# Kernel tuning notes

Measured on AMD Instinct MI355X. Metric: run time of the kernel, lower is better.

## Reference

```python
import jax, jax.numpy as jnp
import numpy as np

B, S, D, A, O = 4, 4096, 256, 64, 256

def setup_inputs() -> dict:
    key = jax.random.key(0)
    k1, k2, k3, k4, k5 = jax.random.split(key, 5)
    x = jax.random.normal(k1, (B, S, D), dtype=jnp.float32)
    # weights stored as [in, out] so projection is x @ W (same math as torch Linear W^T)
    Wk = jax.random.normal(k2, (D, A), dtype=jnp.float32) * (1.0 / np.sqrt(D))
    Wq = jax.random.normal(k3, (D, A), dtype=jnp.float32) * (1.0 / np.sqrt(D))
    Wv = jax.random.normal(k4, (D, A), dtype=jnp.float32) * (1.0 / np.sqrt(D))
    Wo = jax.random.normal(k5, (A, O), dtype=jnp.float32) * (1.0 / np.sqrt(A))
    return {"x": x, "Wk": Wk, "Wq": Wq, "Wv": Wv, "Wo": Wo}

def reference(x, Wk, Wq, Wv, Wo):
    # Single-head self-attention; dropout is identity at inference.
    k = x @ Wk  # [B,S,A]
    q = x @ Wq  # [B,S,A]
    v = x @ Wv  # [B,S,A]
    scale = 1.0 / jnp.sqrt(jnp.asarray(A, x.dtype))
    # logits[b,s,t] = k[b,s,:] . q[b,t,:]   (K @ Q^T in the torch code)
    logits = jnp.einsum('bsa,bta->bst', k, q) * scale
    w = jax.nn.softmax(logits, axis=-1)  # softmax over t
    # out[b,s,:] = sum_t w[b,s,t] * v[b,t,:]  (equivalent to V @ w^T then transpose)
    attn = jnp.einsum('bst,bta->bsa', w, v)
    return attn @ Wo  # [B,S,O]
```

## Files before the change

### kernel.cpp

```cpp
#include <hip/hip_runtime.h>


#define SQN 4096
#define AN 64
#define ON 256

typedef short bf16x8 __attribute__((ext_vector_type(8)));
typedef float f32x4 __attribute__((ext_vector_type(4)));

__device__ __forceinline__ unsigned short f2bf(float f) {
    unsigned int u = __float_as_uint(f);
    u += 0x7fffu + ((u >> 16) & 1u);
    return (unsigned short)(u >> 16);
}
__device__ __forceinline__ unsigned int cvtpk(float lo, float hi) {
    unsigned int r;
    asm("v_cvt_pk_bf16_f32 %0, %1, %2" : "=v"(r) : "v"(lo), "v"(hi));
    return r;
}
__device__ __forceinline__ float exp2_hw(float x) {
    float r; asm("v_exp_f32 %0, %1" : "=v"(r) : "v"(x)); return r;
}

__global__ __launch_bounds__(256) void k_wtrans(
    const float* __restrict__ Wk, const float* __restrict__ Wq,
    const float* __restrict__ Wv, const float* __restrict__ Wo,
    unsigned short* __restrict__ WT, unsigned short* __restrict__ WoT)
{
    int bidx = blockIdx.x, tid = threadIdx.x;
    if (bidx < 24) {
        int m = bidx >> 3, chunk = bidx & 7;
        const float* src = (m == 0) ? Wk : (m == 1) ? Wq : Wv;
        float scl = (m == 1) ? 0.18033688011112042f : 1.0f;
        unsigned short* dst = WT + (m * 64 + chunk * 8) * 256;
        for (int idx = tid; idx < 8 * 256; idx += 256) {
            int a = chunk * 8 + (idx >> 8), d = idx & 255;
            dst[idx] = f2bf(src[d * 64 + a] * scl);
        }
    } else {
        int chunk = bidx - 24;
        for (int idx = tid; idx < 32 * 64; idx += 256) {
            int o = chunk * 32 + (idx >> 6), a = idx & 63;
            WoT[o * 64 + a] = f2bf(Wo[a * 256 + o]);
        }
    }
}

__global__ __launch_bounds__(256) void k_proj(
    const float* __restrict__ x, const unsigned short* __restrict__ WT,
    unsigned short* __restrict__ Ko, unsigned short* __restrict__ Qo,
    unsigned short* __restrict__ VTo)
{
    __shared__ unsigned short x_lds[32 * 256];
    const int tid = threadIdx.x;
    const int wid = tid >> 6, lane = tid & 63, g = lane >> 4, li = lane & 15;
    const int s0 = blockIdx.x * 32;

    {
        const float4* xs = (const float4*)(x + (size_t)s0 * 256);
        #pragma unroll
        for (int i = 0; i < 8; ++i) {
            int idx4 = i * 256 + tid;
            float4 v = xs[idx4];
            int row = idx4 >> 6, q = idx4 & 63;
            int unit = q >> 1, half = q & 1;
            uint2 u; u.x = cvtpk(v.x, v.y); u.y = cvtpk(v.z, v.w);
            *(uint2*)&x_lds[row * 256 + ((unit ^ (row & 7)) << 3) + half * 4] = u;
        }
    }
    __syncthreads();

    f32x4 acc[3][2] = {};
    #pragma unroll
    for (int dc = 0; dc < 8; ++dc) {
        bf16x8 afr[2];
        #pragma unroll
        for (int sf = 0; sf < 2; ++sf) {
            int ar = sf * 16 + li;
            afr[sf] = *(const bf16x8*)&x_lds[ar * 256 + (((4 * dc + g) ^ (ar & 7)) << 3)];
        }
        #pragma unroll
        for (int c = 0; c < 3; ++c) {
            int wc = (wid * 3 + c) * 16 + li;
            bf16x8 bfr = *(const bf16x8*)&WT[wc * 256 + dc * 32 + 8 * g];
            #pragma unroll
            for (int sf = 0; sf < 2; ++sf)
                acc[c][sf] = __builtin_amdgcn_mfma_f32_16x16x32_bf16(afr[sf], bfr, acc[c][sf], 0, 0, 0);
        }
    }

    const int b = s0 >> 12;
    #pragma unroll
    for (int c = 0; c < 3; ++c) {
        int cfg = wid * 3 + c;
        int p = cfg >> 2, col = (cfg & 3) * 16 + li;
        if (p == 2) {
            #pragma unroll
            for (int sf = 0; sf < 2; ++sf) {
                int sb = (s0 & 4095) + sf * 16 + 4 * g;
                uint2 u;
                u.x = cvtpk(acc[c][sf][0], acc[c][sf][1]);
                u.y = cvtpk(acc[c][sf][2], acc[c][sf][3]);
                *(uint2*)&VTo[(((size_t)(b * 64 + col)) << 12) + sb] = u;
            }
        } else {
            unsigned short* dst = (p == 0) ? Ko : Qo;
            #pragma unroll
            for (int sf = 0; sf < 2; ++sf)
                #pragma unroll
                for (int r = 0; r < 4; ++r)
                    dst[(size_t)(s0 + sf * 16 + 4 * g + r) * 64 + col] = f2bf(acc[c][sf][r]);
        }
    }
}

__global__ __launch_bounds__(256) void k_attn(
    const unsigned short* __restrict__ Qg, const unsigned short* __restrict__ Kg,
    const unsigned short* __restrict__ VTg,
    float* __restrict__ Opart, float* __restrict__ Mb, float* __restrict__ Lb)
{
    __shared__ unsigned short q_lds[2][64 * 64];
    __shared__ unsigned short v_lds[2][64 * 64];
    __shared__ unsigned int   p_lds[4][16 * 32];
    const int tid = threadIdx.x;
    const int wid = tid >> 6, lane = tid & 63, g = lane >> 4, li = lane & 15;
    const int b = blockIdx.x >> 8;
    const int s0 = ((blockIdx.x >> 2) & 63) * 64;
    const int h = blockIdx.x & 3;
    const int t_beg = h * 1024;
    const size_t base = (size_t)b * SQN * AN;
    const int srow = tid >> 2, sseg = tid & 3, r7 = srow & 7;
    const int l7 = li & 7;

    bf16x8 kfrag[2];
    {
        const unsigned short* kp = Kg + base + (size_t)(s0 + wid * 16 + li) * 64;
        kfrag[0] = *(const bf16x8*)(kp + 8 * g);
        kfrag[1] = *(const bf16x8*)(kp + 32 + 8 * g);
    }

    {
        const uint4* qs = (const uint4*)(Qg + base + (size_t)(t_beg + srow) * 64 + sseg * 16);
        const uint4* vs = (const uint4*)(VTg + (((size_t)(b * 64 + srow)) << 12) + t_beg + sseg * 16);
        uint4 q0 = qs[0], q1 = qs[1], v0 = vs[0], v1 = vs[1];
        *(uint4*)&q_lds[0][srow * 64 + (((2 * sseg) ^ r7) << 3)] = q0;
        *(uint4*)&q_lds[0][srow * 64 + (((2 * sseg + 1) ^ r7) << 3)] = q1;
        *(uint4*)&v_lds[0][srow * 64 + (((2 * sseg) ^ r7) << 3)] = v0;
        *(uint4*)&v_lds[0][srow * 64 + (((2 * sseg + 1) ^ r7) << 3)] = v1;
    }
    __syncthreads();

    f32x4 ot[4] = {};
    float m_run = -1e30f, l_run = 0.0f;
    int cur = 0;

    for (int ti = 0; ti < 16; ++ti) {
        uint4 qr0, qr1, vr0, vr1;
        const bool pf = (ti < 15);
        if (pf) {
            int t1 = t_beg + (ti + 1) * 64;
            const uint4* qs = (const uint4*)(Qg + base + (size_t)(t1 + srow) * 64 + sseg * 16);
            const uint4* vs = (const uint4*)(VTg + (((size_t)(b * 64 + srow)) << 12) + t1 + sseg * 16);
            qr0 = qs[0]; qr1 = qs[1]; vr0 = vs[0]; vr1 = vs[1];
        }

        f32x4 st[4];
        #pragma unroll
        for (int tf = 0; tf < 4; ++tf) {
            f32x4 a0 = {};
            int qr = tf * 16 + li;
            bf16x8 qa0 = *(const bf16x8*)&q_lds[cur][qr * 64 + ((g ^ l7) << 3)];
            bf16x8 qa1 = *(const bf16x8*)&q_lds[cur][qr * 64 + (((4 + g) ^ l7) << 3)];
            a0 = __builtin_amdgcn_mfma_f32_16x16x32_bf16(qa0, kfrag[0], a0, 0, 0, 0);
            a0 = __builtin_amdgcn_mfma_f32_16x16x32_bf16(qa1, kfrag[1], a0, 0, 0, 0);
            st[tf] = a0;
        }

        float tm = -1e30f;
        #pragma unroll
        for (int tf = 0; tf < 4; ++tf)
            #pragma unroll
            for (int r = 0; r < 4; ++r) tm = fmaxf(tm, st[tf][r]);
        tm = fmaxf(tm, __shfl_xor(tm, 16));
        tm = fmaxf(tm, __shfl_xor(tm, 32));
        if (__any(tm > m_run + 8.0f)) {
            float m_new = fmaxf(m_run, tm);
            float alpha = exp2_hw(m_run - m_new);
            #pragma unroll
            for (int af = 0; af < 4; ++af)
                #pragma unroll
                for (int r = 0; r < 4; ++r) ot[af][r] *= alpha;
            l_run *= alpha;
            m_run = m_new;
        }
        float ts = 0.0f;
        #pragma unroll
        for (int tf = 0; tf < 4; ++tf) {
            float p0 = exp2_hw(st[tf][0] - m_run);
            float p1 = exp2_hw(st[tf][1] - m_run);
            float p2 = exp2_hw(st[tf][2] - m_run);
            float p3 = exp2_hw(st[tf][3] - m_run);
            ts += (p0 + p1) + (p2 + p3);
            uint2 u; u.x = cvtpk(p0, p1); u.y = cvtpk(p2, p3);
            int wi = 8 * tf + 2 * g;
            *(uint2*)&p_lds[wid][li * 32 + (wi ^ (l7 << 2))] = u;
        }
        ts += __shfl_xor(ts, 16);
        ts += __shfl_xor(ts, 32);
        l_run += ts;

        #pragma unroll
        for (int kc = 0; kc < 2; ++kc) {
            uint4 pw = *(const uint4*)&p_lds[wid][li * 32 + ((16 * kc + 4 * g) ^ (l7 << 2))];
            union { uint4 u; bf16x8 v; } pb; pb.u = pw;
            #pragma unroll
            for (int af = 0; af < 4; ++af) {
                int vr = af * 16 + li;
                bf16x8 va = *(const bf16x8*)&v_lds[cur][vr * 64 + (((4 * kc + g) ^ (vr & 7)) << 3)];
                ot[af] = __builtin_amdgcn_mfma_f32_16x16x32_bf16(va, pb.v, ot[af], 0, 0, 0);
            }
        }

        __syncthreads();
        if (pf) {
            *(uint4*)&q_lds[cur ^ 1][srow * 64 + (((2 * sseg) ^ r7) << 3)] = qr0;
            *(uint4*)&q_lds[cur ^ 1][srow * 64 + (((2 * sseg + 1) ^ r7) << 3)] = qr1;
            *(uint4*)&v_lds[cur ^ 1][srow * 64 + (((2 * sseg) ^ r7) << 3)] = vr0;
            *(uint4*)&v_lds[cur ^ 1][srow * 64 + (((2 * sseg + 1) ^ r7) << 3)] = vr1;
        }
        __syncthreads();
        cur ^= 1;
    }

    const int s = s0 + wid * 16 + li;
    float* op = Opart + ((size_t)((h * 4 + b) * 4096 + s)) * 64;
    #pragma unroll
    for (int af = 0; af < 4; ++af) {
        float4 o;
        o.x = ot[af][0]; o.y = ot[af][1]; o.z = ot[af][2]; o.w = ot[af][3];
        *(float4*)(op + af * 16 + 4 * g) = o;
    }
    if (g == 0) {
        Mb[(h * 4 + b) * 4096 + s] = m_run;
        Lb[(h * 4 + b) * 4096 + s] = l_run;
    }
}

__global__ __launch_bounds__(256) void k_combine_oproj(
    const float* __restrict__ Opart, const float* __restrict__ Mb, const float* __restrict__ Lb,
    const unsigned short* __restrict__ WoT, float* __restrict__ out)
{
    __shared__ unsigned short a_lds[16 * 64];
    const int tid = threadIdx.x;
    const int b = blockIdx.x >> 8;
    const int s0 = (blockIdx.x & 255) * 16;

    {
        int row = tid >> 4, ac = (tid & 15) * 4;
        size_t ridx = (size_t)b * 4096 + s0 + row;
        float mm[4], ll[4];
        #pragma unroll
        for (int hh = 0; hh < 4; ++hh) { mm[hh] = Mb[hh * 16384 + ridx]; ll[hh] = Lb[hh * 16384 + ridx]; }
        float M = fmaxf(fmaxf(mm[0], mm[1]), fmaxf(mm[2], mm[3]));
        float w[4], denom = 0.0f;
        #pragma unroll
        for (int hh = 0; hh < 4; ++hh) { w[hh] = exp2_hw(mm[hh] - M); denom += w[hh] * ll[hh]; }
        float inv = 1.0f / denom;
        float4 av = {0.f, 0.f, 0.f, 0.f};
        #pragma unroll
        for (int hh = 0; hh < 4; ++hh) {
            float4 v = *(const float4*)&Opart[((size_t)hh * 16384 + ridx) * 64 + ac];
            av.x += w[hh] * v.x; av.y += w[hh] * v.y; av.z += w[hh] * v.z; av.w += w[hh] * v.w;
        }
        int unit = ac >> 3;
        uint2 u; u.x = cvtpk(av.x * inv, av.y * inv); u.y = cvtpk(av.z * inv, av.w * inv);
        *(uint2*)&a_lds[row * 64 + ((unit ^ (row & 7)) << 3) + (ac & 7)] = u;
    }
    __syncthreads();

    const int wid = tid >> 6, lane = tid & 63, g = lane >> 4, li = lane & 15;
    bf16x8 b0 = *(const bf16x8*)&a_lds[li * 64 + ((g ^ (li & 7)) << 3)];
    bf16x8 b1 = *(const bf16x8*)&a_lds[li * 64 + (((4 + g) ^ (li & 7)) << 3)];
    #pragma unroll
    for (int of = 0; of < 4; ++of) {
        const unsigned short* wp = WoT + (size_t)(wid * 64 + of * 16 + li) * 64;
        bf16x8 w0 = *(const bf16x8*)(wp + 8 * g);
        bf16x8 w1 = *(const bf16x8*)(wp + 32 + 8 * g);
        f32x4 acc = {};
        acc = __builtin_amdgcn_mfma_f32_16x16x32_bf16(w0, b0, acc, 0, 0, 0);
        acc = __builtin_amdgcn_mfma_f32_16x16x32_bf16(w1, b1, acc, 0, 0, 0);
        float4 o;
        o.x = acc[0]; o.y = acc[1]; o.z = acc[2]; o.w = acc[3];
        *(float4*)&out[((size_t)b * 4096 + s0 + li) * 256 + wid * 64 + of * 16 + 4 * g] = o;
    }
}

extern "C" void kernel_launch(void* const* d_in, const int* in_sizes, int n_in,
                              void* d_out, int out_size, void* d_ws, size_t ws_size,
                              hipStream_t stream) {
    const float* x  = (const float*)d_in[0];
    const float* Wk = (const float*)d_in[1];
    const float* Wq = (const float*)d_in[2];
    const float* Wv = (const float*)d_in[3];
    const float* Wo = (const float*)d_in[4];
    float* out = (float*)d_out;

    char* ws = (char*)d_ws;
    unsigned short* WT  = (unsigned short*)(ws);
    unsigned short* WoT = (unsigned short*)(ws + 98304);
    unsigned short* Qb  = (unsigned short*)(ws + 131072);
    unsigned short* Kb  = (unsigned short*)(ws + 131072 + (1u<<21));
    unsigned short* VTb = (unsigned short*)(ws + 131072 + (2u<<21));
    float* Opart = (float*)(ws + 131072 + (3u<<21));
    float* Mb    = (float*)(ws + 131072 + (3u<<21) + (16u<<20));
    float* Lb    = (float*)(ws + 131072 + (3u<<21) + (17u<<20));

    k_wtrans<<<32, 256, 0, stream>>>(Wk, Wq, Wv, Wo, WT, WoT);
    k_proj<<<512, 256, 0, stream>>>(x, WT, Kb, Qb, VTb);
    k_attn<<<1024, 256, 0, stream>>>(Qb, Kb, VTb, Opart, Mb, Lb);
    k_combine_oproj<<<1024, 256, 0, stream>>>(Opart, Mb, Lb, WoT, out);
}
```

Before: 126.7 us.

## Fuse split-KV combine and output projection into 1024-thread attention blocks

Each block now holds 16 waves, four groups of four, and each group handles one quarter of the key range for the same 64 query rows. The partial outputs and max/sum statistics are merged in LDS and fed straight into the Wo projection, so the separate combine kernel and the global Opart/M/L round trip go away. The KV loop now steps through 32-row tiles with a 4-deep LDS ring and register prefetch, and the LDS swizzles change. In exchange the grid drops to 256 large blocks, which may lower occupancy and makes the block-wide barriers per tile more costly.

Result: faster. 122.4 us (-3.4%).

```diff
diff --git a/kernel.cpp b/kernel.cpp
--- a/kernel.cpp
+++ b/kernel.cpp
@@ -3,7 +3,6 @@
 
 #define SQN 4096
 #define AN 64
-#define ON 256
 
 typedef short bf16x8 __attribute__((ext_vector_type(8)));
 typedef float f32x4 __attribute__((ext_vector_type(4)));
@@ -114,163 +113,171 @@
     }
 }
 
-__global__ __launch_bounds__(256) void k_attn(
+__global__ __launch_bounds__(1024, 4) void k_attn(
     const unsigned short* __restrict__ Qg, const unsigned short* __restrict__ Kg,
-    const unsigned short* __restrict__ VTg,
-    float* __restrict__ Opart, float* __restrict__ Mb, float* __restrict__ Lb)
+    const unsigned short* __restrict__ VTg, const unsigned short* __restrict__ WoT,
+    float* __restrict__ out)
 {
-    __shared__ unsigned short q_lds[2][64 * 64];
-    __shared__ unsigned short v_lds[2][64 * 64];
-    __shared__ unsigned int   p_lds[4][16 * 32];
+    __shared__ unsigned short q_lds[4][4][2048];
+    __shared__ unsigned short v_lds[4][4][2048];
+    __shared__ unsigned int   p_lds[16][256];
+
     const int tid = threadIdx.x;
     const int wid = tid >> 6, lane = tid & 63, g = lane >> 4, li = lane & 15;
-    const int b = blockIdx.x >> 8;
-    const int s0 = ((blockIdx.x >> 2) & 63) * 64;
-    const int h = blockIdx.x & 3;
-    const int t_beg = h * 1024;
+    const int grp = wid >> 2, ws = wid & 3;
+    const int b = blockIdx.x >> 6;
+    const int s0 = (blockIdx.x & 63) * 64;
+    const int t_beg = grp * 1024;
     const size_t base = (size_t)b * SQN * AN;
-    const int srow = tid >> 2, sseg = tid & 3, r7 = srow & 7;
-    const int l7 = li & 7;
+
+    const int gtid = tid & 255;
+    const int qrow = gtid >> 3, qseg = gtid & 7;
+    const int vrow = gtid >> 2, vseg = gtid & 3;
+    const int q_woff = qrow * 64 + ((qseg ^ (qrow & 7)) << 3);
+    const int v_woff = vrow * 32 + (((vseg + ((vrow >> 1) & 3)) & 3) << 3);
+    const unsigned short* qg0 = Qg + base + (size_t)(t_beg + qrow) * 64 + qseg * 8;
+    const unsigned short* vg0 = VTg + (((size_t)(b * 64 + vrow)) << 12) + t_beg + vseg * 8;
 
     bf16x8 kfrag[2];
     {
-        const unsigned short* kp = Kg + base + (size_t)(s0 + wid * 16 + li) * 64;
+        const unsigned short* kp = Kg + base + (size_t)(s0 + ws * 16 + li) * 64;
         kfrag[0] = *(const bf16x8*)(kp + 8 * g);
         kfrag[1] = *(const bf16x8*)(kp + 32 + 8 * g);
     }
 
-    {
-        const uint4* qs = (const uint4*)(Qg + base + (size_t)(t_beg + srow) * 64 + sseg * 16);
-        const uint4* vs = (const uint4*)(VTg + (((size_t)(b * 64 + srow)) << 12) + t_beg + sseg * 16);
-        uint4 q0 = qs[0], q1 = qs[1], v0 = vs[0], v1 = vs[1];
-        *(uint4*)&q_lds[0][srow * 64 + (((2 * sseg) ^ r7) << 3)] = q0;
-        *(uint4*)&q_lds[0][srow * 64 + (((2 * sseg + 1) ^ r7) << 3)] = q1;
-        *(uint4*)&v_lds[0][srow * 64 + (((2 * sseg) ^ r7) << 3)] = v0;
-        *(uint4*)&v_lds[0][srow * 64 + (((2 * sseg + 1) ^ r7) << 3)] = v1;
-    }
-    __syncthreads();
-
     f32x4 ot[4] = {};
     float m_run = -1e30f, l_run = 0.0f;
-    int cur = 0;
-
-    for (int ti = 0; ti < 16; ++ti) {
-        uint4 qr0, qr1, vr0, vr1;
-        const bool pf = (ti < 15);
-        if (pf) {
-            int t1 = t_beg + (ti + 1) * 64;
-            const uint4* qs = (const uint4*)(Qg + base + (size_t)(t1 + srow) * 64 + sseg * 16);
-            const uint4* vs = (const uint4*)(VTg + (((size_t)(b * 64 + srow)) << 12) + t1 + sseg * 16);
-            qr0 = qs[0]; qr1 = qs[1]; vr0 = vs[0]; vr1 = vs[1];
-        }
-
-        f32x4 st[4];
-        #pragma unroll
-        for (int tf = 0; tf < 4; ++tf) {
+
+    {
+        uint4 q0 = *(const uint4*)(qg0);
+        uint4 v0 = *(const uint4*)(vg0);
+        *(uint4*)&q_lds[grp][0][q_woff] = q0;
+        *(uint4*)&v_lds[grp][0][v_woff] = v0;
+    }
+    uint4 qsA = *(const uint4*)(qg0 + 2048);
+    uint4 vsA = *(const uint4*)(vg0 + 32);
+    uint4 qsB = {}, vsB = {};
+
+    auto compute = [&](int i) {
+        const unsigned short* qb = &q_lds[grp][i & 3][0];
+        const unsigned short* vb = &v_lds[grp][i & 3][0];
+        f32x4 st[2];
+        #pragma unroll
+        for (int tf = 0; tf < 2; ++tf) {
+            int row = tf * 16 + li;
+            bf16x8 qa0 = *(const bf16x8*)&qb[row * 64 + ((g ^ (row & 7)) << 3)];
+            bf16x8 qa1 = *(const bf16x8*)&qb[row * 64 + (((4 + g) ^ (row & 7)) << 3)];
             f32x4 a0 = {};
-            int qr = tf * 16 + li;
-            bf16x8 qa0 = *(const bf16x8*)&q_lds[cur][qr * 64 + ((g ^ l7) << 3)];
-            bf16x8 qa1 = *(const bf16x8*)&q_lds[cur][qr * 64 + (((4 + g) ^ l7) << 3)];
             a0 = __builtin_amdgcn_mfma_f32_16x16x32_bf16(qa0, kfrag[0], a0, 0, 0, 0);
             a0 = __builtin_amdgcn_mfma_f32_16x16x32_bf16(qa1, kfrag[1], a0, 0, 0, 0);
             st[tf] = a0;
         }
-
-        float tm = -1e30f;
-        #pragma unroll
-        for (int tf = 0; tf < 4; ++tf)
-            #pragma unroll
-            for (int r = 0; r < 4; ++r) tm = fmaxf(tm, st[tf][r]);
+        float tm = fmaxf(fmaxf(fmaxf(st[0][0], st[0][1]), fmaxf(st[0][2], st[0][3])),
+                         fmaxf(fmaxf(st[1][0], st[1][1]), fmaxf(st[1][2], st[1][3])));
         tm = fmaxf(tm, __shfl_xor(tm, 16));
         tm = fmaxf(tm, __shfl_xor(tm, 32));
         if (__any(tm > m_run + 8.0f)) {
             float m_new = fmaxf(m_run, tm);
             float alpha = exp2_hw(m_run - m_new);
             #pragma unroll
-            for (int af = 0; af < 4; ++af)
-                #pragma unroll
-                for (int r = 0; r < 4; ++r) ot[af][r] *= alpha;
+            for (int af = 0; af < 4; ++af) {
+                ot[af][0] *= alpha; ot[af][1] *= alpha;
+                ot[af][2] *= alpha; ot[af][3] *= alpha;
+            }
             l_run *= alpha;
             m_run = m_new;
         }
         float ts = 0.0f;
         #pragma unroll
-        for (int tf = 0; tf < 4; ++tf) {
+        for (int tf = 0; tf < 2; ++tf) {
             float p0 = exp2_hw(st[tf][0] - m_run);
             float p1 = exp2_hw(st[tf][1] - m_run);
             float p2 = exp2_hw(st[tf][2] - m_run);
             float p3 = exp2_hw(st[tf][3] - m_run);
             ts += (p0 + p1) + (p2 + p3);
             uint2 u; u.x = cvtpk(p0, p1); u.y = cvtpk(p2, p3);
-            int wi = 8 * tf + 2 * g;
-            *(uint2*)&p_lds[wid][li * 32 + (wi ^ (l7 << 2))] = u;
+            int w0 = 8 * tf + 2 * g;
+            int su = ((w0 >> 2) + ((li >> 1) & 3)) & 3;
+            *(uint2*)&p_lds[wid][li * 16 + (su << 2) + (w0 & 3)] = u;
         }
         ts += __shfl_xor(ts, 16);
         ts += __shfl_xor(ts, 32);
         l_run += ts;
-
-        #pragma unroll
-        for (int kc = 0; kc < 2; ++kc) {
-            uint4 pw = *(const uint4*)&p_lds[wid][li * 32 + ((16 * kc + 4 * g) ^ (l7 << 2))];
-            union { uint4 u; bf16x8 v; } pb; pb.u = pw;
-            #pragma unroll
-            for (int af = 0; af < 4; ++af) {
-                int vr = af * 16 + li;
-                bf16x8 va = *(const bf16x8*)&v_lds[cur][vr * 64 + (((4 * kc + g) ^ (vr & 7)) << 3)];
-                ot[af] = __builtin_amdgcn_mfma_f32_16x16x32_bf16(va, pb.v, ot[af], 0, 0, 0);
-            }
-        }
-
-        __syncthreads();
-        if (pf) {
-            *(uint4*)&q_lds[cur ^ 1][srow * 64 + (((2 * sseg) ^ r7) << 3)] = qr0;
-            *(uint4*)&q_lds[cur ^ 1][srow * 64 + (((2 * sseg + 1) ^ r7) << 3)] = qr1;
-            *(uint4*)&v_lds[cur ^ 1][srow * 64 + (((2 * sseg) ^ r7) << 3)] = vr0;
-            *(uint4*)&v_lds[cur ^ 1][srow * 64 + (((2 * sseg + 1) ^ r7) << 3)] = vr1;
-        }
-        __syncthreads();
-        cur ^= 1;
-    }
-
-    const int s = s0 + wid * 16 + li;
-    float* op = Opart + ((size_t)((h * 4 + b) * 4096 + s)) * 64;
-    #pragma unroll
-    for (int af = 0; af < 4; ++af) {
-        float4 o;
-        o.x = ot[af][0]; o.y = ot[af][1]; o.z = ot[af][2]; o.w = ot[af][3];
-        *(float4*)(op + af * 16 + 4 * g) = o;
-    }
-    if (g == 0) {
-        Mb[(h * 4 + b) * 4096 + s] = m_run;
-        Lb[(h * 4 + b) * 4096 + s] = l_run;
-    }
-}
-
-__global__ __launch_bounds__(256) void k_combine_oproj(
-    const float* __restrict__ Opart, const float* __restrict__ Mb, const float* __restrict__ Lb,
-    const unsigned short* __restrict__ WoT, float* __restrict__ out)
-{
-    __shared__ unsigned short a_lds[16 * 64];
-    const int tid = threadIdx.x;
-    const int b = blockIdx.x >> 8;
-    const int s0 = (blockIdx.x & 255) * 16;
+        union { uint4 u4; bf16x8 v; } pb;
+        pb.u4 = *(const uint4*)&p_lds[wid][li * 16 + (((g + ((li >> 1) & 3)) & 3) << 2)];
+        #pragma unroll
+        for (int af = 0; af < 4; ++af) {
+            int row = af * 16 + li;
+            bf16x8 va = *(const bf16x8*)&vb[row * 32 + (((g + ((row >> 1) & 3)) & 3) << 3)];
+            ot[af] = __builtin_amdgcn_mfma_f32_16x16x32_bf16(va, pb.v, ot[af], 0, 0, 0);
+        }
+    };
+
+    for (int i = 0; i < 32; i += 2) {
+        {
+            *(uint4*)&q_lds[grp][(i + 1) & 3][q_woff] = qsA;
+            *(uint4*)&v_lds[grp][(i + 1) & 3][v_woff] = vsA;
+            if (i < 30) {
+                qsB = *(const uint4*)(qg0 + (size_t)(i + 2) * 2048);
+                vsB = *(const uint4*)(vg0 + (i + 2) * 32);
+            }
+            __syncthreads();
+            compute(i);
+        }
+        {
+            if (i + 1 < 31) {
+                *(uint4*)&q_lds[grp][(i + 2) & 3][q_woff] = qsB;
+                *(uint4*)&v_lds[grp][(i + 2) & 3][v_woff] = vsB;
+            }
+            if (i + 1 < 30) {
+                qsA = *(const uint4*)(qg0 + (size_t)(i + 3) * 2048);
+                vsA = *(const uint4*)(vg0 + (i + 3) * 32);
+            }
+            __syncthreads();
+            compute(i + 1);
+        }
+    }
+
+    __syncthreads();
+    float* o_part = (float*)&q_lds[0][0][0];
+    float* ml = (float*)&p_lds[0][0];
+    unsigned short* a_lds = (unsigned short*)(ml + 512);
+
+    {
+        int s_loc = ws * 16 + li;
+        float* op = o_part + (size_t)(grp * 64 + s_loc) * 64;
+        #pragma unroll
+        for (int af = 0; af < 4; ++af) {
+            int lu = 4 * af + g;
+            float4 o;
+            o.x = ot[af][0]; o.y = ot[af][1]; o.z = ot[af][2]; o.w = ot[af][3];
+            *(float4*)(op + ((lu ^ (s_loc & 7)) << 2)) = o;
+        }
+        if (g == 0) {
+            ml[grp * 64 + s_loc] = m_run;
+            ml[256 + grp * 64 + s_loc] = l_run;
+        }
+    }
+    __syncthreads();
 
     {
         int row = tid >> 4, ac = (tid & 15) * 4;
-        size_t ridx = (size_t)b * 4096 + s0 + row;
         float mm[4], ll[4];
         #pragma unroll
-        for (int hh = 0; hh < 4; ++hh) { mm[hh] = Mb[hh * 16384 + ridx]; ll[hh] = Lb[hh * 16384 + ridx]; }
+        for (int h = 0; h < 4; ++h) {
+            mm[h] = ml[h * 64 + row];
+            ll[h] = ml[256 + h * 64 + row];
+        }
         float M = fmaxf(fmaxf(mm[0], mm[1]), fmaxf(mm[2], mm[3]));
         float w[4], denom = 0.0f;
         #pragma unroll
-        for (int hh = 0; hh < 4; ++hh) { w[hh] = exp2_hw(mm[hh] - M); denom += w[hh] * ll[hh]; }
+        for (int h = 0; h < 4; ++h) { w[h] = exp2_hw(mm[h] - M); denom += w[h] * ll[h]; }
         float inv = 1.0f / denom;
         float4 av = {0.f, 0.f, 0.f, 0.f};
         #pragma unroll
-        for (int hh = 0; hh < 4; ++hh) {
-            float4 v = *(const float4*)&Opart[((size_t)hh * 16384 + ridx) * 64 + ac];
-            av.x += w[hh] * v.x; av.y += w[hh] * v.y; av.z += w[hh] * v.z; av.w += w[hh] * v.w;
+        for (int h = 0; h < 4; ++h) {
+            float4 v = *(const float4*)&o_part[(size_t)(h * 64 + row) * 64 + (((ac >> 2) ^ (row & 7)) << 2)];
+            av.x += w[h] * v.x; av.y += w[h] * v.y; av.z += w[h] * v.z; av.w += w[h] * v.w;
         }
         int unit = ac >> 3;
         uint2 u; u.x = cvtpk(av.x * inv, av.y * inv); u.y = cvtpk(av.z * inv, av.w * inv);
@@ -278,20 +285,22 @@
     }
     __syncthreads();
 
-    const int wid = tid >> 6, lane = tid & 63, g = lane >> 4, li = lane & 15;
-    bf16x8 b0 = *(const bf16x8*)&a_lds[li * 64 + ((g ^ (li & 7)) << 3)];
-    bf16x8 b1 = *(const bf16x8*)&a_lds[li * 64 + (((4 + g) ^ (li & 7)) << 3)];
-    #pragma unroll
-    for (int of = 0; of < 4; ++of) {
-        const unsigned short* wp = WoT + (size_t)(wid * 64 + of * 16 + li) * 64;
-        bf16x8 w0 = *(const bf16x8*)(wp + 8 * g);
-        bf16x8 w1 = *(const bf16x8*)(wp + 32 + 8 * g);
-        f32x4 acc = {};
-        acc = __builtin_amdgcn_mfma_f32_16x16x32_bf16(w0, b0, acc, 0, 0, 0);
-        acc = __builtin_amdgcn_mfma_f32_16x16x32_bf16(w1, b1, acc, 0, 0, 0);
-        float4 o;
-        o.x = acc[0]; o.y = acc[1]; o.z = acc[2]; o.w = acc[3];
-        *(float4*)&out[((size_t)b * 4096 + s0 + li) * 256 + wid * 64 + of * 16 + 4 * g] = o;
+    {
+        int row = grp * 16 + li;
+        bf16x8 b0 = *(const bf16x8*)&a_lds[row * 64 + ((g ^ (row & 7)) << 3)];
+        bf16x8 b1 = *(const bf16x8*)&a_lds[row * 64 + (((4 + g) ^ (row & 7)) << 3)];
+        #pragma unroll
+        for (int of = 0; of < 4; ++of) {
+            const unsigned short* wp = WoT + (size_t)(ws * 64 + of * 16 + li) * 64;
+            bf16x8 w0 = *(const bf16x8*)(wp + 8 * g);
+            bf16x8 w1 = *(const bf16x8*)(wp + 32 + 8 * g);
+            f32x4 acc = {};
+            acc = __builtin_amdgcn_mfma_f32_16x16x32_bf16(w0, b0, acc, 0, 0, 0);
+            acc = __builtin_amdgcn_mfma_f32_16x16x32_bf16(w1, b1, acc, 0, 0, 0);
+            float4 o;
+            o.x = acc[0]; o.y = acc[1]; o.z = acc[2]; o.w = acc[3];
+            *(float4*)&out[((size_t)b * 4096 + s0 + grp * 16 + li) * 256 + ws * 64 + of * 16 + 4 * g] = o;
+        }
     }
 }
 
@@ -311,12 +320,8 @@
     unsigned short* Qb  = (unsigned short*)(ws + 131072);
     unsigned short* Kb  = (unsigned short*)(ws + 131072 + (1u<<21));
     unsigned short* VTb = (unsigned short*)(ws + 131072 + (2u<<21));
-    float* Opart = (float*)(ws + 131072 + (3u<<21));
-    float* Mb    = (float*)(ws + 131072 + (3u<<21) + (16u<<20));
-    float* Lb    = (float*)(ws + 131072 + (3u<<21) + (17u<<20));
 
     k_wtrans<<<32, 256, 0, stream>>>(Wk, Wq, Wv, Wo, WT, WoT);
     k_proj<<<512, 256, 0, stream>>>(x, WT, Kb, Qb, VTb);
-    k_attn<<<1024, 256, 0, stream>>>(Qb, Kb, VTb, Opart, Mb, Lb);
-    k_combine_oproj<<<1024, 256, 0, stream>>>(Opart, Mb, Lb, WoT, out);
-}
+    k_attn<<<256, 1024, 0, stream>>>(Qb, Kb, VTb, WoT, out);
+}
```
